# Kernel tuning notes

Measured on AMD Instinct MI355X. Metric: run time of the kernel, lower is better.

## Reference

```python
import jax, jax.numpy as jnp
import numpy as np

N, S, E, HEADS = 8, 2048, 1024, 16


def setup_inputs() -> dict:
    root = jax.random.key(0)
    k1, k2, k3, k4, k5, k6 = jax.random.split(root, 6)
    query = jax.random.normal(k1, (N, S, E), jnp.float32)
    key_t = jax.random.normal(k2, (N, S, E), jnp.float32)
    value = jax.random.normal(k3, (N, S, E), jnp.float32)
    # mask broadcasts against the (buggy) energy tensor of shape (N, S, H, H)
    mask = jax.random.randint(k4, (1, 1, HEADS, HEADS), 0, 2, jnp.int32)
    # guarantee no all-masked softmax row (avoid NaN)
    diag = jnp.arange(HEADS)
    mask = mask.at[0, 0, diag, diag].set(1)
    W_out = jax.random.normal(k5, (E, E), jnp.float32) / np.float32(np.sqrt(E))
    b_out = jax.random.normal(k6, (E,), jnp.float32) * 0.02
    return {"query": query, "key": key_t, "value": value, "mask": mask,
            "W_out": W_out, "b_out": b_out, "heads": HEADS}


def reference(query, key, value, mask, W_out, b_out, heads):
    # Faithful translation of the original forward, INCLUDING its einsum-label
    # bug: tensors are transposed to (N, H, S, D) but the einsum subscripts
    # treat axis 1 as 'q/k' and axis 2 as 'h', so softmax runs over heads.
    n, q_len, e = query.shape
    d = e // heads
    inv_scale = np.float32(1.0 / np.sqrt(d))
    q = query.reshape(n, q_len, heads, d).transpose(0, 2, 1, 3)   # (N,H,S,D)
    k = key.reshape(n, q_len, heads, d).transpose(0, 2, 1, 3)     # (N,H,S,D)
    v = value.reshape(n, q_len, heads, d).transpose(0, 2, 1, 3)   # (N,H,S,D)
    # labels applied to transposed tensors -> energy shape (N, S, H, H)
    energy = jnp.einsum('nqhd,nkhd->nhqk', q, k) * inv_scale
    energy = jnp.where(mask == 0, -jnp.inf, energy)
    attention = jax.nn.softmax(energy, axis=-1)                   # over heads axis
    out = jnp.einsum('nhql,nlhd->nqhd', attention, v)             # (N,H,S,D)
    out = out.reshape(n, q_len, e)                                # raw memory reinterp, as torch does
    return out @ W_out.T + b_out
```

## Files before the change

### kernel.cpp

```cpp
#include <hip/hip_runtime.h>
#include <stdint.h>

#define S_LEN 2048
#define EMB 1024

typedef __bf16 bf16x8 __attribute__((ext_vector_type(8)));
typedef __bf16 bf16x4 __attribute__((ext_vector_type(4)));
typedef float f32x4 __attribute__((ext_vector_type(4)));

__device__ __forceinline__ unsigned short f2bf(float f) {
  unsigned int b = __float_as_uint(f);
  b += 0x7FFFu + ((b >> 16) & 1u);
  return (unsigned short)(b >> 16);
}

__device__ __forceinline__ bf16x8 cvt8(float4 a, float4 b) {
  bf16x8 r;
  r[0] = (__bf16)a.x; r[1] = (__bf16)a.y; r[2] = (__bf16)a.z; r[3] = (__bf16)a.w;
  r[4] = (__bf16)b.x; r[5] = (__bf16)b.y; r[6] = (__bf16)b.z; r[7] = (__bf16)b.w;
  return r;
}

#define GLD16(gp, lp)                                                          \
  __builtin_amdgcn_global_load_lds(                                            \
      (const __attribute__((address_space(1))) void*)(gp),                     \
      (__attribute__((address_space(3))) void*)(lp), 16, 0, 0)

__global__ __launch_bounds__(256) void attn_kernel(
    const float* __restrict__ Q, const float* __restrict__ K,
    const float* __restrict__ V, const int* __restrict__ mask,
    __bf16* __restrict__ X) {
  __shared__ __bf16 As[4][2][16][16];

  const int lane = threadIdx.x & 63;
  const int wv = threadIdx.x >> 6;
  const int pos0 = blockIdx.x * 8 + wv * 2;
  const int n = pos0 >> 11;
  const int s0 = pos0 & 2047;
  const int col = lane & 15;
  const int grp = lane >> 4;
  const int gc = grp & 1;
  const int fo = col * 64 + grp * 8;

  const int4 mrow = *(const int4*)(mask + col * 16 + grp * 4);

  float4 qraw[2][4], kraw[2][4];
#pragma unroll
  for (int q = 0; q < 2; ++q) {
    const float* qrow = Q + (size_t)(pos0 + q) * EMB;
    const float* krow = K + (size_t)(pos0 + q) * EMB;
#pragma unroll
    for (int t = 0; t < 2; ++t) {
      qraw[q][t * 2 + 0] = *(const float4*)(qrow + fo + t * 32);
      qraw[q][t * 2 + 1] = *(const float4*)(qrow + fo + t * 32 + 4);
      kraw[q][t * 2 + 0] = *(const float4*)(krow + fo + t * 32);
      kraw[q][t * 2 + 1] = *(const float4*)(krow + fo + t * 32 + 4);
    }
  }
  __builtin_amdgcn_sched_barrier(0);

  float vraw[2][4][8];
#pragma unroll
  for (int q = 0; q < 2; ++q) {
    const float* vrow = V + (size_t)(pos0 + q) * EMB;
#pragma unroll
    for (int c = 0; c < 4; ++c)
#pragma unroll
      for (int e = 0; e < 8; ++e)
        vraw[q][c][e] = vrow[(gc * 8 + e) * 64 + c * 16 + col];
  }
  __builtin_amdgcn_sched_barrier(0);

  f32x4 en[2];
#pragma unroll
  for (int q = 0; q < 2; ++q) {
    const bf16x8 qa0 = cvt8(qraw[q][0], qraw[q][1]);
    const bf16x8 qa1 = cvt8(qraw[q][2], qraw[q][3]);
    const bf16x8 kb0 = cvt8(kraw[q][0], kraw[q][1]);
    const bf16x8 kb1 = cvt8(kraw[q][2], kraw[q][3]);
    f32x4 e = {0.f, 0.f, 0.f, 0.f};
    e = __builtin_amdgcn_mfma_f32_16x16x32_bf16(kb0, qa0, e, 0, 0, 0);
    e = __builtin_amdgcn_mfma_f32_16x16x32_bf16(kb1, qa1, e, 0, 0, 0);
    en[q] = e;
  }

#pragma unroll
  for (int q = 0; q < 2; ++q) {
    float p[4];
    p[0] = (mrow.x == 0) ? -1e30f : en[q][0] * 0.125f;
    p[1] = (mrow.y == 0) ? -1e30f : en[q][1] * 0.125f;
    p[2] = (mrow.z == 0) ? -1e30f : en[q][2] * 0.125f;
    p[3] = (mrow.w == 0) ? -1e30f : en[q][3] * 0.125f;
    float mx = fmaxf(fmaxf(p[0], p[1]), fmaxf(p[2], p[3]));
    mx = fmaxf(mx, __shfl_xor(mx, 16));
    mx = fmaxf(mx, __shfl_xor(mx, 32));
    float ex[4], sm = 0.f;
#pragma unroll
    for (int r = 0; r < 4; ++r) {
      ex[r] = __expf(p[r] - mx);
      sm += ex[r];
    }
    sm += __shfl_xor(sm, 16);
    sm += __shfl_xor(sm, 32);
    const float inv = __builtin_amdgcn_rcpf(sm);
    bf16x4 aw;
#pragma unroll
    for (int r = 0; r < 4; ++r) aw[r] = (__bf16)(ex[r] * inv);
    *(bf16x4*)&As[wv][q][col][grp * 4] = aw;
  }

#pragma unroll
  for (int q = 0; q < 2; ++q) {
    const bf16x8 pt = *(const bf16x8*)&As[wv][q][col][gc * 8];
    bf16x8 pa;
#pragma unroll
    for (int e = 0; e < 8; ++e) pa[e] = (grp < 2) ? pt[e] : (__bf16)0.f;

    const int s = s0 + q;
    const size_t xrow = (size_t)n * S_LEN + (size_t)col * 128 + (s >> 4);
    __bf16* xp = X + xrow * EMB + (size_t)((s & 15) * 64 + grp * 4);
#pragma unroll
    for (int c = 0; c < 4; ++c) {
      bf16x8 vf;
#pragma unroll
      for (int e = 0; e < 8; ++e) vf[e] = (__bf16)vraw[q][c][e];
      f32x4 o = {0.f, 0.f, 0.f, 0.f};
      o = __builtin_amdgcn_mfma_f32_16x16x32_bf16(vf, pa, o, 0, 0, 0);
      bf16x4 w;
#pragma unroll
      for (int r = 0; r < 4; ++r) w[r] = (__bf16)o[r];
      *(bf16x4*)(xp + c * 16) = w;
    }
  }
}

__global__ __launch_bounds__(256) void wconv_kernel(
    const float* __restrict__ W, unsigned short* __restrict__ Wb) {
  const int idx = blockIdx.x * 256 + threadIdx.x;
  float4 w = *(const float4*)(W + (size_t)idx * 4);
  ushort4 o;
  o.x = f2bf(w.x);
  o.y = f2bf(w.y);
  o.z = f2bf(w.z);
  o.w = f2bf(w.w);
  *(ushort4*)(Wb + (size_t)idx * 4) = o;
}

__global__ __launch_bounds__(256) void gemm_kernel(
    const unsigned short* __restrict__ A, const unsigned short* __restrict__ B,
    const float* __restrict__ bias, float* __restrict__ C) {
  __shared__ unsigned short sA[128 * 32];
  __shared__ unsigned short sB[128 * 32];

  int bid = blockIdx.x;
  const int cpx = gridDim.x >> 3;
  bid = (bid & 7) * cpx + (bid >> 3);
  const int tileM = (bid >> 3) * 128;
  const int tileN = (bid & 7) * 128;

  const int t = threadIdx.x;
  const int lane = t & 63;
  const int wid = t >> 6;
  const int wm = wid >> 1, wn = wid & 1;
  const int lrow = lane & 15;
  const int lgrp = lane >> 4;

  f32x4 acc[4][4];
#pragma unroll
  for (int a = 0; a < 4; ++a)
#pragma unroll
    for (int b = 0; b < 4; ++b) acc[a][b] = (f32x4){0.f, 0.f, 0.f, 0.f};

  const int row0 = t >> 2;
  const int kk = (t & 3) * 8;
  const size_t abase = ((size_t)(tileM + row0)) * 1024 + kk;
  const size_t bbase = ((size_t)(tileN + row0)) * 1024 + kk;

  for (int k0 = 0; k0 < 1024; k0 += 32) {
#pragma unroll
    for (int c = 0; c < 2; ++c) {
      GLD16(A + abase + (size_t)c * 64 * 1024 + k0,
            (char*)sA + c * 4096 + t * 16);
      GLD16(B + bbase + (size_t)c * 64 * 1024 + k0,
            (char*)sB + c * 4096 + t * 16);
    }
    __syncthreads();

    bf16x8 af[4], bfr[4];
#pragma unroll
    for (int mi = 0; mi < 4; ++mi)
      af[mi] = *(const bf16x8*)&sA[(wm * 64 + mi * 16 + lrow) * 32 + lgrp * 8];
#pragma unroll
    for (int ni = 0; ni < 4; ++ni)
      bfr[ni] = *(const bf16x8*)&sB[(wn * 64 + ni * 16 + lrow) * 32 + lgrp * 8];
#pragma unroll
    for (int mi = 0; mi < 4; ++mi)
#pragma unroll
      for (int ni = 0; ni < 4; ++ni)
        acc[mi][ni] = __builtin_amdgcn_mfma_f32_16x16x32_bf16(
            af[mi], bfr[ni], acc[mi][ni], 0, 0, 0);
    __syncthreads();
  }

#pragma unroll
  for (int ni = 0; ni < 4; ++ni) {
    const int colc = tileN + wn * 64 + ni * 16 + lrow;
    const float bv = bias[colc];
#pragma unroll
    for (int mi = 0; mi < 4; ++mi) {
      const int row = tileM + wm * 64 + mi * 16 + lgrp * 4;
#pragma unroll
      for (int r = 0; r < 4; ++r)
        C[(size_t)(row + r) * 1024 + colc] = acc[mi][ni][r] + bv;
    }
  }
}

extern "C" void kernel_launch(void* const* d_in, const int* in_sizes, int n_in,
                              void* d_out, int out_size, void* d_ws,
                              size_t ws_size, hipStream_t stream) {
  const float* Q = (const float*)d_in[0];
  const float* K = (const float*)d_in[1];
  const float* V = (const float*)d_in[2];
  const int* mask = (const int*)d_in[3];
  const float* W = (const float*)d_in[4];
  const float* bias = (const float*)d_in[5];
  float* out = (float*)d_out;

  __bf16* X = (__bf16*)d_ws;
  unsigned short* Wb =
      (unsigned short*)((char*)d_ws + (size_t)32 * 1024 * 1024);

  hipLaunchKernelGGL(attn_kernel, dim3(8 * S_LEN / 8), dim3(256), 0, stream,
                     Q, K, V, mask, X);
  hipLaunchKernelGGL(wconv_kernel, dim3(1024), dim3(256), 0, stream, W, Wb);
  hipLaunchKernelGGL(gemm_kernel, dim3(1024), dim3(256), 0, stream,
                     (const unsigned short*)X, Wb, bias, out);
}
```

Baseline: 99.38 us.

## Stage Q/K/V through LDS with coalesced loads and coalesced output writes

The attention kernel now loads the block's eight positions of Q, K and V with fully coalesced float4 loads. It converts them to bf16 and stores them in swizzled shared memory, and the MFMA operands are read back from LDS. This replaces the strided per-lane global loads, in particular the scattered scalar V gathers. Outputs are staged in a padded LDS buffer and written to X as contiguous 16-byte chunks. The cost is a larger LDS footprint, which may lower occupancy, plus two block-wide barriers.

```diff
diff --git a/kernel.cpp b/kernel.cpp
--- a/kernel.cpp
+++ b/kernel.cpp
@@ -14,10 +14,9 @@
   return (unsigned short)(b >> 16);
 }
 
-__device__ __forceinline__ bf16x8 cvt8(float4 a, float4 b) {
-  bf16x8 r;
+__device__ __forceinline__ bf16x4 c4(float4 a) {
+  bf16x4 r;
   r[0] = (__bf16)a.x; r[1] = (__bf16)a.y; r[2] = (__bf16)a.z; r[3] = (__bf16)a.w;
-  r[4] = (__bf16)b.x; r[5] = (__bf16)b.y; r[6] = (__bf16)b.z; r[7] = (__bf16)b.w;
   return r;
 }
 
@@ -30,54 +29,51 @@
     const float* __restrict__ Q, const float* __restrict__ K,
     const float* __restrict__ V, const int* __restrict__ mask,
     __bf16* __restrict__ X) {
-  __shared__ __bf16 As[4][2][16][16];
-
-  const int lane = threadIdx.x & 63;
-  const int wv = threadIdx.x >> 6;
-  const int pos0 = blockIdx.x * 8 + wv * 2;
+  __shared__ __bf16 Qb[8][1024];
+  __shared__ __bf16 Kb[8][1024];
+  __shared__ __bf16 Vb[8][1024];
+  __shared__ __bf16 As[8][16][16];
+  __shared__ __bf16 Ob[8 * 1160];
+
+  const int t = threadIdx.x;
+  const int lane = t & 63;
+  const int wv = t >> 6;
+  const int pos0 = blockIdx.x * 8;
   const int n = pos0 >> 11;
   const int s0 = pos0 & 2047;
   const int col = lane & 15;
   const int grp = lane >> 4;
   const int gc = grp & 1;
-  const int fo = col * 64 + grp * 8;
 
   const int4 mrow = *(const int4*)(mask + col * 16 + grp * 4);
 
-  float4 qraw[2][4], kraw[2][4];
+  {
+    const float* qsrc = Q + (size_t)pos0 * EMB;
+    const float* ksrc = K + (size_t)pos0 * EMB;
+    const float* vsrc = V + (size_t)pos0 * EMB;
+    const int bsw = (t * 8) ^ (((t >> 4) & 7) << 4);
+#pragma unroll
+    for (int i = 0; i < 8; ++i) {
+      const float4 qv = *(const float4*)(qsrc + i * 1024 + t * 4);
+      const float4 kv = *(const float4*)(ksrc + i * 1024 + t * 4);
+      const float4 vv = *(const float4*)(vsrc + i * 1024 + t * 4);
+      *(bf16x4*)((char*)&Qb[i][0] + bsw) = c4(qv);
+      *(bf16x4*)((char*)&Kb[i][0] + bsw) = c4(kv);
+      *(bf16x4*)&Vb[i][t * 4] = c4(vv);
+    }
+  }
+  __syncthreads();
+
+  const int fb0 = (col * 128 + grp * 16) ^ ((col & 7) << 4);
+  const int fb1 = (col * 128 + grp * 16 + 64) ^ ((col & 7) << 4);
+  f32x4 en[2];
 #pragma unroll
   for (int q = 0; q < 2; ++q) {
-    const float* qrow = Q + (size_t)(pos0 + q) * EMB;
-    const float* krow = K + (size_t)(pos0 + q) * EMB;
-#pragma unroll
-    for (int t = 0; t < 2; ++t) {
-      qraw[q][t * 2 + 0] = *(const float4*)(qrow + fo + t * 32);
-      qraw[q][t * 2 + 1] = *(const float4*)(qrow + fo + t * 32 + 4);
-      kraw[q][t * 2 + 0] = *(const float4*)(krow + fo + t * 32);
-      kraw[q][t * 2 + 1] = *(const float4*)(krow + fo + t * 32 + 4);
-    }
-  }
-  __builtin_amdgcn_sched_barrier(0);
-
-  float vraw[2][4][8];
-#pragma unroll
-  for (int q = 0; q < 2; ++q) {
-    const float* vrow = V + (size_t)(pos0 + q) * EMB;
-#pragma unroll
-    for (int c = 0; c < 4; ++c)
-#pragma unroll
-      for (int e = 0; e < 8; ++e)
-        vraw[q][c][e] = vrow[(gc * 8 + e) * 64 + c * 16 + col];
-  }
-  __builtin_amdgcn_sched_barrier(0);
-
-  f32x4 en[2];
-#pragma unroll
-  for (int q = 0; q < 2; ++q) {
-    const bf16x8 qa0 = cvt8(qraw[q][0], qraw[q][1]);
-    const bf16x8 qa1 = cvt8(qraw[q][2], qraw[q][3]);
-    const bf16x8 kb0 = cvt8(kraw[q][0], kraw[q][1]);
-    const bf16x8 kb1 = cvt8(kraw[q][2], kraw[q][3]);
+    const int pl = wv * 2 + q;
+    const bf16x8 qa0 = *(const bf16x8*)((const char*)&Qb[pl][0] + fb0);
+    const bf16x8 qa1 = *(const bf16x8*)((const char*)&Qb[pl][0] + fb1);
+    const bf16x8 kb0 = *(const bf16x8*)((const char*)&Kb[pl][0] + fb0);
+    const bf16x8 kb1 = *(const bf16x8*)((const char*)&Kb[pl][0] + fb1);
     f32x4 e = {0.f, 0.f, 0.f, 0.f};
     e = __builtin_amdgcn_mfma_f32_16x16x32_bf16(kb0, qa0, e, 0, 0, 0);
     e = __builtin_amdgcn_mfma_f32_16x16x32_bf16(kb1, qa1, e, 0, 0, 0);
@@ -86,6 +82,7 @@
 
 #pragma unroll
   for (int q = 0; q < 2; ++q) {
+    const int pl = wv * 2 + q;
     float p[4];
     p[0] = (mrow.x == 0) ? -1e30f : en[q][0] * 0.125f;
     p[1] = (mrow.y == 0) ? -1e30f : en[q][1] * 0.125f;
@@ -106,31 +103,40 @@
     bf16x4 aw;
 #pragma unroll
     for (int r = 0; r < 4; ++r) aw[r] = (__bf16)(ex[r] * inv);
-    *(bf16x4*)&As[wv][q][col][grp * 4] = aw;
-  }
-
-#pragma unroll
-  for (int q = 0; q < 2; ++q) {
-    const bf16x8 pt = *(const bf16x8*)&As[wv][q][col][gc * 8];
+    *(bf16x4*)&As[pl][col][grp * 4] = aw;
+
+    const bf16x8 pt = *(const bf16x8*)&As[pl][col][gc * 8];
     bf16x8 pa;
 #pragma unroll
     for (int e = 0; e < 8; ++e) pa[e] = (grp < 2) ? pt[e] : (__bf16)0.f;
 
-    const int s = s0 + q;
-    const size_t xrow = (size_t)n * S_LEN + (size_t)col * 128 + (s >> 4);
-    __bf16* xp = X + xrow * EMB + (size_t)((s & 15) * 64 + grp * 4);
+    __bf16* ob = &Ob[pl * 1160];
 #pragma unroll
     for (int c = 0; c < 4; ++c) {
       bf16x8 vf;
 #pragma unroll
-      for (int e = 0; e < 8; ++e) vf[e] = (__bf16)vraw[q][c][e];
+      for (int e = 0; e < 8; ++e)
+        vf[e] = Vb[pl][(gc * 8 + e) * 64 + c * 16 + col];
       f32x4 o = {0.f, 0.f, 0.f, 0.f};
       o = __builtin_amdgcn_mfma_f32_16x16x32_bf16(vf, pa, o, 0, 0, 0);
       bf16x4 w;
 #pragma unroll
       for (int r = 0; r < 4; ++r) w[r] = (__bf16)o[r];
-      *(bf16x4*)(xp + c * 16) = w;
-    }
+      *(bf16x4*)(ob + col * 72 + c * 16 + grp * 4) = w;
+    }
+  }
+  __syncthreads();
+
+#pragma unroll
+  for (int it = 0; it < 4; ++it) {
+    const int chunk = it * 256 + t;
+    const int i = chunk >> 6;
+    const int off = (chunk & 63) * 8;
+    const int pl = off >> 6;
+    const int d0 = off & 63;
+    const bf16x8 v = *(const bf16x8*)&Ob[pl * 1160 + i * 72 + d0];
+    const size_t row = (size_t)n * S_LEN + (size_t)i * 128 + (s0 >> 4);
+    *(bf16x8*)&X[row * EMB + (size_t)((s0 & 15) * 64 + off)] = v;
   }
 }
 
```

After: 97.61 us. No clear change (-1.8%).
